# Optimization experiments

Hardware: AMD Instinct MI355X
Metric: run time of the kernel (lower is better)

Reference implementation:

```python
import jax, jax.numpy as jnp
import numpy as np

N, E, IN, H, C, OUT = 50000, 800000, 128, 4, 32, 40
HID = H * C  # 128


def _layernorm(x, g, b, eps=1e-5):
    mu = x.mean(-1, keepdims=True)
    var = ((x - mu) ** 2).mean(-1, keepdims=True)
    return (x - mu) * jax.lax.rsqrt(var + eps) * g + b


def _gatv2(x, src, dst, Wl, bl, Wr, br, att, bias, heads, ch, concat):
    n = x.shape[0]
    xl = (x @ Wl + bl).reshape(n, heads, ch)  # source-side transform
    xr = (x @ Wr + br).reshape(n, heads, ch)  # target-side transform
    e = jax.nn.leaky_relu(xl[src] + xr[dst], 0.2)          # [E,H,C]
    alpha = jnp.einsum('ehc,hc->eh', e, att)                # [E,H]
    m = jax.ops.segment_max(alpha, dst, num_segments=n)
    m = jnp.where(jnp.isfinite(m), m, 0.0)
    a = jnp.exp(alpha - m[dst])
    denom = jax.ops.segment_sum(a, dst, num_segments=n)
    a = a / (denom[dst] + 1e-16)
    out = jax.ops.segment_sum(xl[src] * a[:, :, None], dst, num_segments=n)  # [N,H,C]
    out = out.reshape(n, heads * ch) if concat else out.mean(1)
    return out + bias


def setup_inputs():
    key = jax.random.key(0)
    ks = jax.random.split(key, 26)
    s = 0.05
    rn = lambda k, sh: jax.random.normal(k, sh, jnp.float32) * s
    inp = {
        'x': jax.random.normal(ks[0], (N, IN), jnp.float32),
        'edge_index': jax.random.randint(ks[1], (2, E), 0, N, jnp.int64),
        'W0': rn(ks[2], (IN, HID)), 'b0': jnp.zeros((HID,), jnp.float32),
        'W1l': rn(ks[3], (IN, HID)), 'b1l': jnp.zeros((HID,), jnp.float32),
        'W1r': rn(ks[4], (IN, HID)), 'b1r': jnp.zeros((HID,), jnp.float32),
        'att1': rn(ks[5], (H, C)), 'bias1': jnp.zeros((HID,), jnp.float32),
        'g1': jnp.ones((HID,), jnp.float32), 'be1': jnp.zeros((HID,), jnp.float32),
        'W2l': rn(ks[6], (HID, HID)), 'b2l': jnp.zeros((HID,), jnp.float32),
        'W2r': rn(ks[7], (HID, HID)), 'b2r': jnp.zeros((HID,), jnp.float32),
        'att2': rn(ks[8], (H, C)), 'bias2': jnp.zeros((HID,), jnp.float32),
        'g2': jnp.ones((HID,), jnp.float32), 'be2': jnp.zeros((HID,), jnp.float32),
        'W3l': rn(ks[9], (HID, OUT)), 'b3l': jnp.zeros((OUT,), jnp.float32),
        'W3r': rn(ks[10], (HID, OUT)), 'b3r': jnp.zeros((OUT,), jnp.float32),
        'att3': rn(ks[11], (1, OUT)), 'bias3': jnp.zeros((OUT,), jnp.float32),
    }
    return inp


def reference(x, edge_index, W0, b0, W1l, b1l, W1r, b1r, att1, bias1, g1, be1,
              W2l, b2l, W2r, b2r, att2, bias2, g2, be2,
              W3l, b3l, W3r, b3r, att3, bias3):
    src, dst = edge_index[0], edge_index[1]
    identity = x @ W0 + b0
    out = _gatv2(x, src, dst, W1l, b1l, W1r, b1r, att1, bias1, H, C, True)
    out = jax.nn.gelu(_layernorm(out, g1, be1), approximate=False)
    x1 = out + identity  # dropout is identity in eval mode
    out = _gatv2(x1, src, dst, W2l, b2l, W2r, b2r, att2, bias2, H, C, True)
    out = jax.nn.gelu(_layernorm(out, g2, be2), approximate=False)
    x2 = out + x1
    return _gatv2(x2, src, dst, W3l, b3l, W3r, b3r, att3, bias3, 1, OUT, False)
```

## Files before the change

### kernel.cpp

```cpp
#include <hip/hip_runtime.h>
#include <hip/hip_bf16.h>

#define NN 50000
#define EE 800000
#define OUTD 40
#define NBUCK 196
#define BCAP 8192
#define ABLKS 400
#define EPB 2000

typedef __attribute__((ext_vector_type(8))) short short8;
typedef __attribute__((ext_vector_type(4))) float floatx4;

__device__ __forceinline__ float bf2f(unsigned short u) {
  union { unsigned int i; float f; } v; v.i = ((unsigned int)u) << 16; return v.f;
}
__device__ __forceinline__ unsigned short f2bf(float f) {
  union { float f; unsigned int i; } v; v.f = f;
  unsigned int x = v.i;
  return (unsigned short)((x + 0x7fffu + ((x >> 16) & 1u)) >> 16);
}
__device__ __forceinline__ float blo(unsigned int u) {
  union { unsigned int i; float f; } v; v.i = u << 16; return v.f;
}
__device__ __forceinline__ float bhi(unsigned int u) {
  union { unsigned int i; float f; } v; v.i = u & 0xffff0000u; return v.f;
}

template <int CTRL>
__device__ __forceinline__ float dpp_add(float x) {
  int y = __builtin_amdgcn_update_dpp(0, __float_as_int(x), CTRL, 0xF, 0xF, true);
  return x + __int_as_float(y);
}

__device__ __forceinline__ float gelu1(float y) {
  float y2 = y * y;
  float z = y * fmaf(0.0356774081f, y2, 0.7978845608f);
  float e = __expf(-2.f * z);
  float r = __builtin_amdgcn_rcpf(1.f + e);
  float th = fmaf(2.f, r, -1.f);
  return y * fmaf(0.5f, th, 0.5f);
}

__device__ __forceinline__ int clampe(int i, int last) {
  int r = i <= last ? i : last;
  return r < 0 ? 0 : r;
}

__device__ __forceinline__ int probe_f32(const void* x) {
  int lane = threadIdx.x & 63;
  unsigned short u = ((const unsigned short*)x)[2 * lane];
  int exf = (u >> 7) & 0xFF;
  unsigned long long b = __ballot((exf >= 100 && exf <= 142) ? 1 : 0);
  return (__popcll(b) >= 48) ? 0 : 1;
}
__device__ __forceinline__ int probe_i64(const void* ei) {
  int lane = threadIdx.x & 63;
  long long v = ((const long long*)ei)[lane];
  unsigned long long b = __ballot((v >= 0 && v < NN) ? 1 : 0);
  return (__popcll(b) >= 48) ? 1 : 0;
}

struct WDesc { const void* W; unsigned short* F; int T; int ncols; };
struct WDescs { WDesc d[7]; int cum[8]; };
struct PCv { const void* s; unsigned short* d; int n; int cap; };
struct PCvs { PCv a[17]; };

struct GSet { const unsigned short* F; const unsigned short* bias; unsigned short* Out; };
struct GArgs { GSet s[3]; };

__device__ __forceinline__ short8 pack_f4(float4 u0, float4 u1) {
  short8 r;
  r[0] = (short)f2bf(u0.x); r[1] = (short)f2bf(u0.y);
  r[2] = (short)f2bf(u0.z); r[3] = (short)f2bf(u0.w);
  r[4] = (short)f2bf(u1.x); r[5] = (short)f2bf(u1.y);
  r[6] = (short)f2bf(u1.z); r[7] = (short)f2bf(u1.w);
  return r;
}

__device__ __forceinline__ void gemm_body(int wave, int lane, const void* __restrict__ A,
                                          int f32, const GArgs& g, int nset, int M,
                                          int T, int ncols) {
  int r0 = wave * 16;
  if (r0 >= M) return;
  int m = lane & 15, quad = lane >> 4;
  short8 a0, a1, a2, a3;
  if (!f32) {
    const unsigned short* ar = (const unsigned short*)A + (size_t)(r0 + m) * 128 + quad * 8;
    a0 = *(const short8*)(ar);
    a1 = *(const short8*)(ar + 32);
    a2 = *(const short8*)(ar + 64);
    a3 = *(const short8*)(ar + 96);
  } else {
    const float* ar = (const float*)A + (size_t)(r0 + m) * 128 + quad * 8;
    a0 = pack_f4(*(const float4*)(ar), *(const float4*)(ar + 4));
    a1 = pack_f4(*(const float4*)(ar + 32), *(const float4*)(ar + 36));
    a2 = pack_f4(*(const float4*)(ar + 64), *(const float4*)(ar + 68));
    a3 = pack_f4(*(const float4*)(ar + 96), *(const float4*)(ar + 100));
  }
  size_t kstride = (size_t)T * 64 * 8;
  for (int si = 0; si < nset; ++si) {
    const unsigned short* F = g.s[si].F;
    const unsigned short* bias = g.s[si].bias;
    unsigned short* Out = g.s[si].Out;
    for (int t = 0; t < T; ++t) {
      floatx4 acc = {0.f, 0.f, 0.f, 0.f};
      const unsigned short* wp = F + ((size_t)t * 64 + lane) * 8;
      acc = __builtin_amdgcn_mfma_f32_16x16x32_bf16(a0, *(const short8*)(wp), acc, 0, 0, 0);
      acc = __builtin_amdgcn_mfma_f32_16x16x32_bf16(a1, *(const short8*)(wp + kstride), acc, 0, 0, 0);
      acc = __builtin_amdgcn_mfma_f32_16x16x32_bf16(a2, *(const short8*)(wp + 2 * kstride), acc, 0, 0, 0);
      acc = __builtin_amdgcn_mfma_f32_16x16x32_bf16(a3, *(const short8*)(wp + 3 * kstride), acc, 0, 0, 0);
      int col = t * 16 + m;
      if (col < ncols) {
        float bb = bf2f(bias[col]);
        for (int r = 0; r < 4; ++r) {
          int row = r0 + quad * 4 + r;
          Out[(size_t)row * ncols + col] = f2bf(acc[r] + bb);
        }
      }
    }
  }
}

__global__ __launch_bounds__(512) void fused_scatter_init(
    const void* __restrict__ ei, const void* __restrict__ x,
    unsigned int* __restrict__ bedges, int* __restrict__ bcur,
    int* __restrict__ flags, WDescs ds, PCvs P) {
  __shared__ int lhist[NBUCK];
  __shared__ int lbase[NBUCK];
  if (blockIdx.x >= ABLKS) {
    int b = blockIdx.x - ABLKS;
    int tid = threadIdx.x;
    int f32 = probe_f32(x);
    if (b < 24) {
      int idx = b * 512 + tid;
      if (idx >= 12288) return;
      int mi = 0;
      while (idx >= ds.cum[mi + 1]) mi++;
      int local = idx - ds.cum[mi];
      WDesc d = ds.d[mi];
      int lane = local & 63;
      int rest = local >> 6;
      int t = rest % d.T;
      int kb = rest / d.T;
      int m = lane & 15, quad = lane >> 4;
      int col = t * 16 + m;
      short8 v;
      for (int j = 0; j < 8; ++j) {
        int k = kb * 32 + quad * 8 + j;
        if (col < d.ncols) {
          int off = k * d.ncols + col;
          v[j] = f32 ? (short)f2bf(((const float*)d.W)[off])
                     : (short)((const unsigned short*)d.W)[off];
        } else {
          v[j] = 0;
        }
      }
      *(short8*)(d.F + (size_t)local * 8) = v;
    } else if (b < 41) {
      PCv p = P.a[b - 24];
      for (int i = tid; i < p.cap; i += 512) {
        unsigned short o = 0;
        if (i < p.n)
          o = f32 ? f2bf(((const float*)p.s)[i]) : ((const unsigned short*)p.s)[i];
        p.d[i] = o;
      }
    } else {
      if (tid < 64) {
        int i64 = probe_i64(ei);
        if (tid == 0) {
          flags[0] = i64;
          flags[1] = f32;
          flags[2] = 0;
        }
      }
    }
    return;
  }
  int tid = threadIdx.x;
  if (tid < NBUCK) lhist[tid] = 0;
  int i64 = probe_i64(ei);
  __syncthreads();
  int e0 = blockIdx.x * EPB;
  int e1 = e0 + EPB; if (e1 > EE) e1 = EE;
  for (int e = e0 + tid; e < e1; e += 512) {
    int d = i64 ? (int)((const long long*)ei)[EE + e] : ((const int*)ei)[EE + e];
    d = d < 0 ? 0 : (d >= NN ? NN - 1 : d);
    atomicAdd(&lhist[d >> 8], 1);
  }
  __syncthreads();
  if (tid < NBUCK) {
    int c = lhist[tid];
    lbase[tid] = c ? atomicAdd(&bcur[tid * 16], c) : 0;
    lhist[tid] = 0;
  }
  __syncthreads();
  for (int e = e0 + tid; e < e1; e += 512) {
    int s, d;
    if (i64) {
      s = (int)((const long long*)ei)[e];
      d = (int)((const long long*)ei)[EE + e];
    } else {
      s = ((const int*)ei)[e];
      d = ((const int*)ei)[EE + e];
    }
    s = s < 0 ? 0 : (s >= NN ? NN - 1 : s);
    d = d < 0 ? 0 : (d >= NN ? NN - 1 : d);
    int bin = d >> 8;
    int r = atomicAdd(&lhist[bin], 1);
    int pos = lbase[bin] + r;
    if (pos < BCAP)
      bedges[(size_t)bin * BCAP + pos] =
          ((unsigned int)(d & 0xFF) << 24) | ((unsigned int)s << 8);
  }
}

__global__ __launch_bounds__(512) void fused_sort_gemm(
    const unsigned int* __restrict__ bedges, const int* __restrict__ bcur,
    int* __restrict__ offs, int* __restrict__ src_sorted,
    const void* __restrict__ A, const int* __restrict__ flagp, GArgs g,
    int nset, int M, int T, int ncols) {
  __shared__ int lhist[256];
  __shared__ int lscan[256];
  __shared__ int lbin[256];
  __shared__ int sbase, scount, stotal;
  __shared__ unsigned int le[BCAP];
  __shared__ unsigned short lrank[BCAP];
  if (blockIdx.x >= NBUCK) {
    int wave = (blockIdx.x - NBUCK) * 8 + (threadIdx.x >> 6);
    gemm_body(wave, threadIdx.x & 63, A, *flagp, g, nset, M, T, ncols);
    return;
  }
  int k = blockIdx.x;
  int tid = threadIdx.x;
  if (tid < 256) {
    int c = 0;
    if (tid < NBUCK) {
      int v = bcur[tid * 16];
      c = v < BCAP ? v : BCAP;
    }
    lscan[tid] = c;
  }
  __syncthreads();
  for (int off = 1; off < 256; off <<= 1) {
    int u = 0;
    if (tid < 256 && tid >= off) u = lscan[tid - off];
    __syncthreads();
    if (tid < 256) lscan[tid] += u;
    __syncthreads();
  }
  if (tid == 0) {
    int pb = (k == 0) ? 0 : lscan[k - 1];
    sbase = pb;
    scount = lscan[k] - pb;
    stotal = lscan[NBUCK - 1];
  }
  if (tid < 256) lhist[tid] = 0;
  __syncthreads();
  int base = sbase, count = scount;
  const unsigned int* myb = bedges + (size_t)k * BCAP;
  for (int i = tid; i < count; i += 512) {
    unsigned int pk = myb[i];
    int bin = pk >> 24;
    int r = atomicAdd(&lhist[bin], 1);
    le[i] = pk;
    lrank[i] = (unsigned short)r;
  }
  __syncthreads();
  int hc = 0;
  if (tid < 256) {
    hc = lhist[tid];
    lscan[tid] = hc;
  }
  __syncthreads();
  for (int off = 1; off < 256; off <<= 1) {
    int u = 0;
    if (tid < 256 && tid >= off) u = lscan[tid - off];
    __syncthreads();
    if (tid < 256) lscan[tid] += u;
    __syncthreads();
  }
  if (tid < 256) {
    int binoff = lscan[tid] - hc;
    lbin[tid] = binoff;
    int node = k * 256 + tid;
    if (node < NN) offs[node] = base + binoff;
    if (k == 0 && tid == 0) offs[NN] = stotal;
  }
  __syncthreads();
  for (int i = tid; i < count; i += 512) {
    unsigned int pk = le[i];
    int bin = pk >> 24;
    int pos = base + lbin[bin] + (int)lrank[i];
    src_sorted[pos] = (int)(pk & 0x00FFFF00u);
  }
}

template <int TT, int NCOLS, int WRITEX>
__global__ __launch_bounds__(512) void edge_hid_kernel(
    const unsigned short* __restrict__ xl, const unsigned short* __restrict__ xr,
    const unsigned short* __restrict__ att, const unsigned short* __restrict__ bias,
    const unsigned short* __restrict__ gamma, const unsigned short* __restrict__ beta,
    const unsigned short* __restrict__ resid, unsigned short* __restrict__ xout,
    const int* __restrict__ offs, const int* __restrict__ srcs,
    const unsigned short* __restrict__ Fl, const unsigned short* __restrict__ Fr,
    const unsigned short* __restrict__ bl, const unsigned short* __restrict__ br,
    unsigned short* __restrict__ outl, unsigned short* __restrict__ outr) {
  __shared__ unsigned short sA[16 * 136];
  const int wid = threadIdx.x >> 6;
  int wpair = blockIdx.x * 8 + wid;
  int lane = threadIdx.x & 63;
  int half = lane >> 5;
  int wv = wpair * 2 + half;
  int hl = lane & 31;
  int sub = hl >> 4;
  int cb = (hl & 15) * 16;
  int beg = offs[wv], end = offs[wv + 1], last = end - 1;
  int iters = (end - beg + 1) >> 1;
  int oi = __shfl_xor(iters, 32);
  int maxit = __builtin_amdgcn_readfirstlane(iters > oi ? iters : oi);
  const char* xlb = (const char*)xl;
  int c0 = hl * 4;
  uint2 rr = *(const uint2*)(resid + (size_t)wv * 128 + c0);
  uint4 xr8 = *(const uint4*)((const char*)xr + (size_t)wv * 256 + cb);
  float rx0 = blo(xr8.x), rx1 = bhi(xr8.x), rx2 = blo(xr8.y), rx3 = bhi(xr8.y);
  float rx4 = blo(xr8.z), rx5 = bhi(xr8.z), rx6 = blo(xr8.w), rx7 = bhi(xr8.w);
  uint4 at8 = *(const uint4*)((const char*)att + cb);
  float a0 = blo(at8.x), a1 = bhi(at8.x), a2 = blo(at8.y), a3 = bhi(at8.y);
  float a4 = blo(at8.z), a5 = bhi(at8.z), a6 = blo(at8.w), a7 = bhi(at8.w);
  float acc0 = 0.f, acc1 = 0.f, acc2 = 0.f, acc3 = 0.f;
  float acc4 = 0.f, acc5 = 0.f, acc6 = 0.f, acc7 = 0.f, den = 0.f;
  int ir = beg + sub;
  int o_cur = srcs[clampe(ir, last)];
  int o_nxt = srcs[clampe(ir + 2, last)];
  uint4 u = *(const uint4*)(xlb + (o_cur + cb));
  for (int it = 0; it < maxit; ++it) {
    int o_p = srcs[clampe(ir + 4, last)];
    uint4 un = *(const uint4*)(xlb + (o_nxt + cb));
    float mk = (ir <= last) ? 1.f : 0.f;
    ir += 2;
    float x0 = blo(u.x), x1 = bhi(u.x), x2 = blo(u.y), x3 = bhi(u.y);
    float x4 = blo(u.z), x5 = bhi(u.z), x6 = blo(u.w), x7 = bhi(u.w);
    float t0 = x0 + rx0, t1 = x1 + rx1, t2 = x2 + rx2, t3 = x3 + rx3;
    float t4 = x4 + rx4, t5 = x5 + rx5, t6 = x6 + rx6, t7 = x7 + rx7;
    float pa = a0 * t0;
    pa = fmaf(a1, t1, pa); pa = fmaf(a2, t2, pa); pa = fmaf(a3, t3, pa);
    pa = fmaf(a4, t4, pa); pa = fmaf(a5, t5, pa); pa = fmaf(a6, t6, pa); pa = fmaf(a7, t7, pa);
    float pb = a0 * fabsf(t0);
    pb = fmaf(a1, fabsf(t1), pb); pb = fmaf(a2, fabsf(t2), pb); pb = fmaf(a3, fabsf(t3), pb);
    pb = fmaf(a4, fabsf(t4), pb); pb = fmaf(a5, fabsf(t5), pb);
    pb = fmaf(a6, fabsf(t6), pb); pb = fmaf(a7, fabsf(t7), pb);
    float p = fmaf(0.4f, pb, 0.6f * pa);
    p = dpp_add<0xB1>(p);
    p = dpp_add<0x4E>(p);
    float w = __expf(fminf(p, 60.f)) * mk;
    den += w;
    acc0 = fmaf(w, x0, acc0); acc1 = fmaf(w, x1, acc1);
    acc2 = fmaf(w, x2, acc2); acc3 = fmaf(w, x3, acc3);
    acc4 = fmaf(w, x4, acc4); acc5 = fmaf(w, x5, acc5);
    acc6 = fmaf(w, x6, acc6); acc7 = fmaf(w, x7, acc7);
    u = un;
    o_nxt = o_p;
  }
  den += __shfl_xor(den, 16);
  acc0 += __shfl_xor(acc0, 16); acc1 += __shfl_xor(acc1, 16);
  acc2 += __shfl_xor(acc2, 16); acc3 += __shfl_xor(acc3, 16);
  acc4 += __shfl_xor(acc4, 16); acc5 += __shfl_xor(acc5, 16);
  acc6 += __shfl_xor(acc6, 16); acc7 += __shfl_xor(acc7, 16);
  int srcLane = (half << 5) + (hl >> 1);
  float b0 = __shfl(acc0, srcLane), b1 = __shfl(acc1, srcLane);
  float b2 = __shfl(acc2, srcLane), b3 = __shfl(acc3, srcLane);
  float h4 = __shfl(acc4, srcLane), h5 = __shfl(acc5, srcLane);
  float h6 = __shfl(acc6, srcLane), h7 = __shfl(acc7, srcLane);
  float dn = __shfl(den, srcLane);
  bool hi = (hl & 1) != 0;
  float v0 = hi ? h4 : b0, v1 = hi ? h5 : b1, v2 = hi ? h6 : b2, v3 = hi ? h7 : b3;
  float inv = __builtin_amdgcn_rcpf(dn + 1e-16f);
  uint2 bb = *(const uint2*)(bias + c0);
  float o0 = v0 * inv + blo(bb.x), o1 = v1 * inv + bhi(bb.x);
  float o2 = v2 * inv + blo(bb.y), o3 = v3 * inv + bhi(bb.y);
  float s = (o0 + o1) + (o2 + o3);
  for (int k = 1; k < 32; k <<= 1) s += __shfl_xor(s, k);
  float mu = s * (1.f / 128.f);
  float d0 = o0 - mu, d1 = o1 - mu, d2 = o2 - mu, d3 = o3 - mu;
  float q = (d0 * d0 + d1 * d1) + (d2 * d2 + d3 * d3);
  for (int k = 1; k < 32; k <<= 1) q += __shfl_xor(q, k);
  float rstd = rsqrtf(q * (1.f / 128.f) + 1e-5f);
  uint2 gg = *(const uint2*)(gamma + c0);
  uint2 be = *(const uint2*)(beta + c0);
  float y0 = d0 * rstd * blo(gg.x) + blo(be.x);
  float y1 = d1 * rstd * bhi(gg.x) + bhi(be.x);
  float y2 = d2 * rstd * blo(gg.y) + blo(be.y);
  float y3 = d3 * rstd * bhi(gg.y) + bhi(be.y);
  y0 = gelu1(y0); y1 = gelu1(y1); y2 = gelu1(y2); y3 = gelu1(y3);
  y0 += blo(rr.x); y1 += bhi(rr.x); y2 += blo(rr.y); y3 += bhi(rr.y);
  uint2 pk;
  pk.x = (unsigned int)f2bf(y0) | ((unsigned int)f2bf(y1) << 16);
  pk.y = (unsigned int)f2bf(y2) | ((unsigned int)f2bf(y3) << 16);
  if (WRITEX) *(uint2*)(xout + (size_t)wv * 128 + c0) = pk;

  int lrow = wid * 2 + half;
  *(uint2*)(&sA[lrow * 136 + c0]) = pk;
  __syncthreads();
  int m = lane & 15, quad = lane >> 4;
  const unsigned short* arow = sA + m * 136 + quad * 8;
  short8 A0 = *(const short8*)(arow);
  short8 A1 = *(const short8*)(arow + 32);
  short8 A2 = *(const short8*)(arow + 64);
  short8 A3 = *(const short8*)(arow + 96);
  const size_t kst = (size_t)TT * 64 * 8;
  const int rowbase = blockIdx.x * 16;
  constexpr int PER = (2 * TT) / 8;
#pragma unroll
  for (int jj = 0; jj < PER; ++jj) {
    int j = wid * PER + jj;
    bool isr = j >= TT;
    const unsigned short* F = isr ? Fr : Fl;
    const unsigned short* bs = isr ? br : bl;
    unsigned short* Out = isr ? outr : outl;
    int t = isr ? j - TT : j;
    floatx4 acc = {0.f, 0.f, 0.f, 0.f};
    const unsigned short* wp = F + ((size_t)t * 64 + lane) * 8;
    acc = __builtin_amdgcn_mfma_f32_16x16x32_bf16(A0, *(const short8*)(wp), acc, 0, 0, 0);
    acc = __builtin_amdgcn_mfma_f32_16x16x32_bf16(A1, *(const short8*)(wp + kst), acc, 0, 0, 0);
    acc = __builtin_amdgcn_mfma_f32_16x16x32_bf16(A2, *(const short8*)(wp + 2 * kst), acc, 0, 0, 0);
    acc = __builtin_amdgcn_mfma_f32_16x16x32_bf16(A3, *(const short8*)(wp + 3 * kst), acc, 0, 0, 0);
    int col = t * 16 + m;
    float bbv = bf2f(bs[col]);
#pragma unroll
    for (int r = 0; r < 4; ++r)
      Out[(size_t)(rowbase + quad * 4 + r) * NCOLS + col] = f2bf(acc[r] + bbv);
  }
}

__global__ __launch_bounds__(256) void edge_out_kernel(
    const unsigned short* __restrict__ xl, const unsigned short* __restrict__ xr,
    const unsigned short* __restrict__ att, const unsigned short* __restrict__ bias,
    void* __restrict__ out, const int* __restrict__ flagp,
    const int* __restrict__ offs, const int* __restrict__ srcs) {
  int wv = blockIdx.x * 4 + (threadIdx.x >> 6);
  if (wv >= NN) return;
  int lane = threadIdx.x & 63;
  int oct = lane >> 3;
  int cb = (lane & 7) * 16;
  int beg = __builtin_amdgcn_readfirstlane(offs[wv]);
  int last = __builtin_amdgcn_readfirstlane(offs[wv + 1]) - 1;
  const char* xlb = (const char*)xl;
  uint4 xr8 = *(const uint4*)((const char*)xr + (size_t)wv * 128 + cb);
  float rx0 = blo(xr8.x), rx1 = bhi(xr8.x), rx2 = blo(xr8.y), rx3 = bhi(xr8.y);
  float rx4 = blo(xr8.z), rx5 = bhi(xr8.z), rx6 = blo(xr8.w), rx7 = bhi(xr8.w);
  uint4 at8 = *(const uint4*)((const char*)att + cb);
  float a0 = blo(at8.x), a1 = bhi(at8.x), a2 = blo(at8.y), a3 = bhi(at8.y);
  float a4 = blo(at8.z), a5 = bhi(at8.z), a6 = blo(at8.w), a7 = bhi(at8.w);
  float acc0 = 0.f, acc1 = 0.f, acc2 = 0.f, acc3 = 0.f;
  float acc4 = 0.f, acc5 = 0.f, acc6 = 0.f, acc7 = 0.f, den = 0.f;
  int ir = beg + oct;
  int o_cur = srcs[clampe(ir, last)];
  int o_nxt = srcs[clampe(ir + 8, last)];
  uint4 u = *(const uint4*)(xlb + ((o_cur >> 1) + cb));
  for (int e = beg; e <= last; e += 8) {
    int o_p = srcs[clampe(ir + 16, last)];
    uint4 un = *(const uint4*)(xlb + ((o_nxt >> 1) + cb));
    float mk = (ir <= last) ? 1.f : 0.f;
    ir += 8;
    float x0 = blo(u.x), x1 = bhi(u.x), x2 = blo(u.y), x3 = bhi(u.y);
    float x4 = blo(u.z), x5 = bhi(u.z), x6 = blo(u.w), x7 = bhi(u.w);
    float t0 = x0 + rx0, t1 = x1 + rx1, t2 = x2 + rx2, t3 = x3 + rx3;
    float t4 = x4 + rx4, t5 = x5 + rx5, t6 = x6 + rx6, t7 = x7 + rx7;
    float pa = a0 * t0;
    pa = fmaf(a1, t1, pa); pa = fmaf(a2, t2, pa); pa = fmaf(a3, t3, pa);
    pa = fmaf(a4, t4, pa); pa = fmaf(a5, t5, pa); pa = fmaf(a6, t6, pa); pa = fmaf(a7, t7, pa);
    float pb = a0 * fabsf(t0);
    pb = fmaf(a1, fabsf(t1), pb); pb = fmaf(a2, fabsf(t2), pb); pb = fmaf(a3, fabsf(t3), pb);
    pb = fmaf(a4, fabsf(t4), pb); pb = fmaf(a5, fabsf(t5), pb);
    pb = fmaf(a6, fabsf(t6), pb); pb = fmaf(a7, fabsf(t7), pb);
    float p = fmaf(0.4f, pb, 0.6f * pa);
    p = dpp_add<0xB1>(p);
    p = dpp_add<0x4E>(p);
    p = dpp_add<0x141>(p);
    float w = __expf(fminf(p, 60.f)) * mk;
    den += w;
    acc0 = fmaf(w, x0, acc0); acc1 = fmaf(w, x1, acc1);
    acc2 = fmaf(w, x2, acc2); acc3 = fmaf(w, x3, acc3);
    acc4 = fmaf(w, x4, acc4); acc5 = fmaf(w, x5, acc5);
    acc6 = fmaf(w, x6, acc6); acc7 = fmaf(w, x7, acc7);
    u = un;
    o_nxt = o_p;
  }
  den += __shfl_xor(den, 8);  den += __shfl_xor(den, 16);  den += __shfl_xor(den, 32);
  acc0 += __shfl_xor(acc0, 8); acc0 += __shfl_xor(acc0, 16); acc0 += __shfl_xor(acc0, 32);
  acc1 += __shfl_xor(acc1, 8); acc1 += __shfl_xor(acc1, 16); acc1 += __shfl_xor(acc1, 32);
  acc2 += __shfl_xor(acc2, 8); acc2 += __shfl_xor(acc2, 16); acc2 += __shfl_xor(acc2, 32);
  acc3 += __shfl_xor(acc3, 8); acc3 += __shfl_xor(acc3, 16); acc3 += __shfl_xor(acc3, 32);
  acc4 += __shfl_xor(acc4, 8); acc4 += __shfl_xor(acc4, 16); acc4 += __shfl_xor(acc4, 32);
  acc5 += __shfl_xor(acc5, 8); acc5 += __shfl_xor(acc5, 16); acc5 += __shfl_xor(acc5, 32);
  acc6 += __shfl_xor(acc6, 8); acc6 += __shfl_xor(acc6, 16); acc6 += __shfl_xor(acc6, 32);
  acc7 += __shfl_xor(acc7, 8); acc7 += __shfl_xor(acc7, 16); acc7 += __shfl_xor(acc7, 32);
  float inv = __builtin_amdgcn_rcpf(den + 1e-16f);
  if (lane < 5) {
    uint4 bb = *(const uint4*)((const char*)bias + cb);
    float v0 = acc0 * inv + blo(bb.x), v1 = acc1 * inv + bhi(bb.x);
    float v2 = acc2 * inv + blo(bb.y), v3 = acc3 * inv + bhi(bb.y);
    float v4 = acc4 * inv + blo(bb.z), v5 = acc5 * inv + bhi(bb.z);
    float v6 = acc6 * inv + blo(bb.w), v7 = acc7 * inv + bhi(bb.w);
    int c0 = lane * 8;
    if (*flagp) {
      float* op = (float*)out + (size_t)wv * OUTD + c0;
      float4 f0 = {v0, v1, v2, v3};
      float4 f1 = {v4, v5, v6, v7};
      *(float4*)(op) = f0;
      *(float4*)(op + 4) = f1;
    } else {
      uint4 pk;
      pk.x = (unsigned int)f2bf(v0) | ((unsigned int)f2bf(v1) << 16);
      pk.y = (unsigned int)f2bf(v2) | ((unsigned int)f2bf(v3) << 16);
      pk.z = (unsigned int)f2bf(v4) | ((unsigned int)f2bf(v5) << 16);
      pk.w = (unsigned int)f2bf(v6) | ((unsigned int)f2bf(v7) << 16);
      *(uint4*)((unsigned short*)out + (size_t)wv * OUTD + c0) = pk;
    }
  }
}

extern "C" void kernel_launch(void* const* d_in, const int* in_sizes, int n_in,
                              void* d_out, int out_size, void* d_ws, size_t ws_size,
                              hipStream_t stream) {
  const void* x = d_in[0];
  const void* ei = d_in[1];

  char* ws = (char*)d_ws;
  size_t o = 0;
  auto alloc = [&](size_t bytes) {
    void* p = ws + o;
    o = (o + bytes + 255) & ~(size_t)255;
    return p;
  };
  int* flags = (int*)alloc(256);
  int* src_sorted = (int*)alloc((size_t)EE * 4);
  int* offs = (int*)alloc((size_t)(NN + 1) * 4);
  int* bcur = (int*)alloc((size_t)NBUCK * 16 * 4);
  unsigned int* bedges = (unsigned int*)alloc((size_t)NBUCK * BCAP * 4);
  unsigned short* F_W0 = (unsigned short*)alloc(2048 * 16);
  unsigned short* F_W1l = (unsigned short*)alloc(2048 * 16);
  unsigned short* F_W1r = (unsigned short*)alloc(2048 * 16);
  unsigned short* F_W2l = (unsigned short*)alloc(2048 * 16);
  unsigned short* F_W2r = (unsigned short*)alloc(2048 * 16);
  unsigned short* F_W3l = (unsigned short*)alloc(1024 * 16);
  unsigned short* F_W3r = (unsigned short*)alloc(1024 * 16);
  unsigned short* pblk = (unsigned short*)alloc(4096);
  unsigned short* ident = (unsigned short*)alloc((size_t)NN * 128 * 2);
  unsigned short* bxlA = (unsigned short*)alloc((size_t)NN * 128 * 2);
  unsigned short* bxrA = (unsigned short*)alloc((size_t)NN * 128 * 2);
  unsigned short* bxlB = (unsigned short*)alloc((size_t)NN * 128 * 2);
  unsigned short* bxrB = (unsigned short*)alloc((size_t)NN * 128 * 2);
  (void)ws_size;

  unsigned short* pb0 = pblk;
  unsigned short* pb1l = pblk + 128;
  unsigned short* pb1r = pblk + 256;
  unsigned short* patt1 = pblk + 384;
  unsigned short* pbias1 = pblk + 512;
  unsigned short* pg1 = pblk + 640;
  unsigned short* pbe1 = pblk + 768;
  unsigned short* pb2l = pblk + 896;
  unsigned short* pb2r = pblk + 1024;
  unsigned short* patt2 = pblk + 1152;
  unsigned short* pbias2 = pblk + 1280;
  unsigned short* pg2 = pblk + 1408;
  unsigned short* pbe2 = pblk + 1536;
  unsigned short* pb3l = pblk + 1664;
  unsigned short* pb3r = pblk + 1728;
  unsigned short* patt3 = pblk + 1792;
  unsigned short* pbias3 = pblk + 1856;

  WDescs wd;
  wd.d[0] = {d_in[2], F_W0, 8, 128};
  wd.d[1] = {d_in[4], F_W1l, 8, 128};
  wd.d[2] = {d_in[6], F_W1r, 8, 128};
  wd.d[3] = {d_in[12], F_W2l, 8, 128};
  wd.d[4] = {d_in[14], F_W2r, 8, 128};
  wd.d[5] = {d_in[20], F_W3l, 4, 40};
  wd.d[6] = {d_in[22], F_W3r, 4, 40};
  int cum[8] = {0, 2048, 4096, 6144, 8192, 10240, 11264, 12288};
  for (int i = 0; i < 8; ++i) wd.cum[i] = cum[i];
  PCvs P;
  P.a[0] = {d_in[3], pb0, 128, 128};
  P.a[1] = {d_in[5], pb1l, 128, 128};
  P.a[2] = {d_in[7], pb1r, 128, 128};
  P.a[3] = {d_in[8], patt1, 128, 128};
  P.a[4] = {d_in[9], pbias1, 128, 128};
  P.a[5] = {d_in[10], pg1, 128, 128};
  P.a[6] = {d_in[11], pbe1, 128, 128};
  P.a[7] = {d_in[13], pb2l, 128, 128};
  P.a[8] = {d_in[15], pb2r, 128, 128};
  P.a[9] = {d_in[16], patt2, 128, 128};
  P.a[10] = {d_in[17], pbias2, 128, 128};
  P.a[11] = {d_in[18], pg2, 128, 128};
  P.a[12] = {d_in[19], pbe2, 128, 128};
  P.a[13] = {d_in[21], pb3l, 40, 64};
  P.a[14] = {d_in[23], pb3r, 40, 64};
  P.a[15] = {d_in[24], patt3, 40, 64};
  P.a[16] = {d_in[25], pbias3, 40, 64};

  const int* fx = flags + 1;
  const int gb8 = (NN + 127) / 128;
  const int eb = (NN + 3) / 4;
  const int eb16 = NN / 16;

  hipMemsetAsync(bcur, 0, (size_t)NBUCK * 16 * 4, stream);

  fused_scatter_init<<<ABLKS + 42, 512, 0, stream>>>(ei, x, bedges, bcur, flags, wd, P);

  GArgs g1a;
  g1a.s[0] = {F_W0, pb0, ident};
  g1a.s[1] = {F_W1l, pb1l, bxlA};
  g1a.s[2] = {F_W1r, pb1r, bxrA};
  fused_sort_gemm<<<NBUCK + gb8, 512, 0, stream>>>(bedges, bcur, offs, src_sorted, x,
                                                   fx, g1a, 3, NN, 8, 128);

  edge_hid_kernel<8, 128, 1><<<eb16, 512, 0, stream>>>(
      bxlA, bxrA, patt1, pbias1, pg1, pbe1, ident, ident, offs, src_sorted,
      F_W2l, F_W2r, pb2l, pb2r, bxlB, bxrB);

  edge_hid_kernel<4, 64, 0><<<eb16, 512, 0, stream>>>(
      bxlB, bxrB, patt2, pbias2, pg2, pbe2, ident, ident, offs, src_sorted,
      F_W3l, F_W3r, pb3l, pb3r, bxlA, bxrA);

  edge_out_kernel<<<eb, 256, 0, stream>>>(bxlA, bxrA, patt3, pbias3, d_out, fx, offs,
                                          src_sorted);
}
```

Before: 288.1 us.

## Merge all stages into one cooperative persistent kernel with grid syncs

Replaces five separate kernel launches with a single cooperative mega-kernel that loops over virtual blocks for each phase and separates the phases with grid-wide syncs. Shared memory becomes a union across phases, and the per-bucket capacity is lowered so the larger union fits and more blocks can be resident. The goal is to remove launch gaps and tail effects between stages. In exchange it adds grid-sync cost, puts one shared-memory footprint on every phase, and the smaller bucket capacity could overflow if destination degrees are skewed. The edge-output phase now maps 8 waves per virtual block instead of 4.

```diff
diff --git a/kernel.cpp b/kernel.cpp
--- a/kernel.cpp
+++ b/kernel.cpp
@@ -1,13 +1,21 @@
 #include <hip/hip_runtime.h>
 #include <hip/hip_bf16.h>
+#include <hip/hip_cooperative_groups.h>
+
+namespace cg = cooperative_groups;
 
 #define NN 50000
 #define EE 800000
 #define OUTD 40
 #define NBUCK 196
-#define BCAP 8192
+#define BCAP 4608
 #define ABLKS 400
 #define EPB 2000
+#define GB8 391
+#define NV1 (ABLKS + 42)
+#define NV2 (NBUCK + GB8)
+#define NV3 (NN / 16)
+#define NV5 (NN / 8)
 
 typedef __attribute__((ext_vector_type(8))) short short8;
 typedef __attribute__((ext_vector_type(4))) float floatx4;
@@ -65,9 +73,34 @@
 struct WDescs { WDesc d[7]; int cum[8]; };
 struct PCv { const void* s; unsigned short* d; int n; int cap; };
 struct PCvs { PCv a[17]; };
-
 struct GSet { const unsigned short* F; const unsigned short* bias; unsigned short* Out; };
 struct GArgs { GSet s[3]; };
+
+union SharedU {
+  struct { int lhist[NBUCK]; int lbase[NBUCK]; } s1;
+  struct {
+    int lhist[256]; int lscan[256]; int lbin[256];
+    int sbase, scount, stotal;
+    unsigned int le[BCAP];
+    unsigned short lrank[BCAP];
+  } s2;
+  unsigned short sA[16 * 136];
+};
+
+struct MegaArgs {
+  const void* x; const void* ei;
+  unsigned int* bedges; int* bcur; int* flags;
+  int* offs; int* srcs;
+  WDescs wd; PCvs P;
+  GArgs g1;
+  const unsigned short *patt1, *pbias1, *pg1, *pbe1;
+  const unsigned short *patt2, *pbias2, *pg2, *pbe2;
+  const unsigned short *patt3, *pbias3;
+  const unsigned short *F2l, *F2r, *b2l, *b2r;
+  const unsigned short *F3l, *F3r, *b3l, *b3r;
+  unsigned short *ident, *bxlA, *bxrA, *bxlB, *bxrB;
+  void* out;
+};
 
 __device__ __forceinline__ short8 pack_f4(float4 u0, float4 u1) {
   short8 r;
@@ -78,9 +111,8 @@
   return r;
 }
 
-__device__ __forceinline__ void gemm_body(int wave, int lane, const void* __restrict__ A,
-                                          int f32, const GArgs& g, int nset, int M,
-                                          int T, int ncols) {
+__device__ void gemm_body(int wave, int lane, const void* __restrict__ A,
+                          int f32, const GArgs& g, int nset, int M, int T, int ncols) {
   int r0 = wave * 16;
   if (r0 >= M) return;
   int m = lane & 15, quad = lane >> 4;
@@ -122,23 +154,18 @@
   }
 }
 
-__global__ __launch_bounds__(512) void fused_scatter_init(
-    const void* __restrict__ ei, const void* __restrict__ x,
-    unsigned int* __restrict__ bedges, int* __restrict__ bcur,
-    int* __restrict__ flags, WDescs ds, PCvs P) {
-  __shared__ int lhist[NBUCK];
-  __shared__ int lbase[NBUCK];
-  if (blockIdx.x >= ABLKS) {
-    int b = blockIdx.x - ABLKS;
+__device__ void phase_scatter_init(int vb, SharedU& su, const MegaArgs& a) {
+  if (vb >= ABLKS) {
+    int b = vb - ABLKS;
     int tid = threadIdx.x;
-    int f32 = probe_f32(x);
+    int f32 = probe_f32(a.x);
     if (b < 24) {
       int idx = b * 512 + tid;
       if (idx >= 12288) return;
       int mi = 0;
-      while (idx >= ds.cum[mi + 1]) mi++;
-      int local = idx - ds.cum[mi];
-      WDesc d = ds.d[mi];
+      while (idx >= a.wd.cum[mi + 1]) mi++;
+      int local = idx - a.wd.cum[mi];
+      WDesc d = a.wd.d[mi];
       int lane = local & 63;
       int rest = local >> 6;
       int t = rest % d.T;
@@ -158,7 +185,7 @@
       }
       *(short8*)(d.F + (size_t)local * 8) = v;
     } else if (b < 41) {
-      PCv p = P.a[b - 24];
+      PCv p = a.P.a[b - 24];
       for (int i = tid; i < p.cap; i += 512) {
         unsigned short o = 0;
         if (i < p.n)
@@ -167,32 +194,33 @@
       }
     } else {
       if (tid < 64) {
-        int i64 = probe_i64(ei);
+        int i64 = probe_i64(a.ei);
         if (tid == 0) {
-          flags[0] = i64;
-          flags[1] = f32;
-          flags[2] = 0;
+          a.flags[0] = i64;
+          a.flags[1] = f32;
+          a.flags[2] = 0;
         }
       }
     }
     return;
   }
   int tid = threadIdx.x;
-  if (tid < NBUCK) lhist[tid] = 0;
-  int i64 = probe_i64(ei);
-  __syncthreads();
-  int e0 = blockIdx.x * EPB;
+  if (tid < NBUCK) su.s1.lhist[tid] = 0;
+  int i64 = probe_i64(a.ei);
+  __syncthreads();
+  int e0 = vb * EPB;
   int e1 = e0 + EPB; if (e1 > EE) e1 = EE;
+  const void* ei = a.ei;
   for (int e = e0 + tid; e < e1; e += 512) {
     int d = i64 ? (int)((const long long*)ei)[EE + e] : ((const int*)ei)[EE + e];
     d = d < 0 ? 0 : (d >= NN ? NN - 1 : d);
-    atomicAdd(&lhist[d >> 8], 1);
+    atomicAdd(&su.s1.lhist[d >> 8], 1);
   }
   __syncthreads();
   if (tid < NBUCK) {
-    int c = lhist[tid];
-    lbase[tid] = c ? atomicAdd(&bcur[tid * 16], c) : 0;
-    lhist[tid] = 0;
+    int c = su.s1.lhist[tid];
+    su.s1.lbase[tid] = c ? atomicAdd(&a.bcur[tid * 16], c) : 0;
+    su.s1.lhist[tid] = 0;
   }
   __syncthreads();
   for (int e = e0 + tid; e < e1; e += 512) {
@@ -207,108 +235,107 @@
     s = s < 0 ? 0 : (s >= NN ? NN - 1 : s);
     d = d < 0 ? 0 : (d >= NN ? NN - 1 : d);
     int bin = d >> 8;
-    int r = atomicAdd(&lhist[bin], 1);
-    int pos = lbase[bin] + r;
+    int r = atomicAdd(&su.s1.lhist[bin], 1);
+    int pos = su.s1.lbase[bin] + r;
     if (pos < BCAP)
-      bedges[(size_t)bin * BCAP + pos] =
+      a.bedges[(size_t)bin * BCAP + pos] =
           ((unsigned int)(d & 0xFF) << 24) | ((unsigned int)s << 8);
   }
-}
-
-__global__ __launch_bounds__(512) void fused_sort_gemm(
-    const unsigned int* __restrict__ bedges, const int* __restrict__ bcur,
-    int* __restrict__ offs, int* __restrict__ src_sorted,
-    const void* __restrict__ A, const int* __restrict__ flagp, GArgs g,
-    int nset, int M, int T, int ncols) {
-  __shared__ int lhist[256];
-  __shared__ int lscan[256];
-  __shared__ int lbin[256];
-  __shared__ int sbase, scount, stotal;
-  __shared__ unsigned int le[BCAP];
-  __shared__ unsigned short lrank[BCAP];
-  if (blockIdx.x >= NBUCK) {
-    int wave = (blockIdx.x - NBUCK) * 8 + (threadIdx.x >> 6);
-    gemm_body(wave, threadIdx.x & 63, A, *flagp, g, nset, M, T, ncols);
+  __syncthreads();
+}
+
+__device__ void phase_sort_gemm(int vb, SharedU& su, const MegaArgs& a) {
+  if (vb >= NBUCK) {
+    int wave = (vb - NBUCK) * 8 + (threadIdx.x >> 6);
+    gemm_body(wave, threadIdx.x & 63, a.x, a.flags[1], a.g1, 3, NN, 8, 128);
     return;
   }
-  int k = blockIdx.x;
+  auto& s = su.s2;
+  int k = vb;
   int tid = threadIdx.x;
   if (tid < 256) {
     int c = 0;
     if (tid < NBUCK) {
-      int v = bcur[tid * 16];
+      int v = a.bcur[tid * 16];
       c = v < BCAP ? v : BCAP;
     }
-    lscan[tid] = c;
+    s.lscan[tid] = c;
   }
   __syncthreads();
   for (int off = 1; off < 256; off <<= 1) {
     int u = 0;
-    if (tid < 256 && tid >= off) u = lscan[tid - off];
+    if (tid < 256 && tid >= off) u = s.lscan[tid - off];
     __syncthreads();
-    if (tid < 256) lscan[tid] += u;
+    if (tid < 256) s.lscan[tid] += u;
     __syncthreads();
   }
   if (tid == 0) {
-    int pb = (k == 0) ? 0 : lscan[k - 1];
-    sbase = pb;
-    scount = lscan[k] - pb;
-    stotal = lscan[NBUCK - 1];
-  }
-  if (tid < 256) lhist[tid] = 0;
-  __syncthreads();
-  int base = sbase, count = scount;
-  const unsigned int* myb = bedges + (size_t)k * BCAP;
+    int pb = (k == 0) ? 0 : s.lscan[k - 1];
+    s.sbase = pb;
+    s.scount = s.lscan[k] - pb;
+    s.stotal = s.lscan[NBUCK - 1];
+  }
+  if (tid < 256) s.lhist[tid] = 0;
+  __syncthreads();
+  int base = s.sbase, count = s.scount;
+  const unsigned int* myb = a.bedges + (size_t)k * BCAP;
   for (int i = tid; i < count; i += 512) {
     unsigned int pk = myb[i];
     int bin = pk >> 24;
-    int r = atomicAdd(&lhist[bin], 1);
-    le[i] = pk;
-    lrank[i] = (unsigned short)r;
+    int r = atomicAdd(&s.lhist[bin], 1);
+    s.le[i] = pk;
+    s.lrank[i] = (unsigned short)r;
   }
   __syncthreads();
   int hc = 0;
   if (tid < 256) {
-    hc = lhist[tid];
-    lscan[tid] = hc;
+    hc = s.lhist[tid];
+    s.lscan[tid] = hc;
   }
   __syncthreads();
   for (int off = 1; off < 256; off <<= 1) {
     int u = 0;
-    if (tid < 256 && tid >= off) u = lscan[tid - off];
+    if (tid < 256 && tid >= off) u = s.lscan[tid - off];
     __syncthreads();
-    if (tid < 256) lscan[tid] += u;
+    if (tid < 256) s.lscan[tid] += u;
     __syncthreads();
   }
   if (tid < 256) {
-    int binoff = lscan[tid] - hc;
-    lbin[tid] = binoff;
+    int binoff = s.lscan[tid] - hc;
+    s.lbin[tid] = binoff;
     int node = k * 256 + tid;
-    if (node < NN) offs[node] = base + binoff;
-    if (k == 0 && tid == 0) offs[NN] = stotal;
+    if (node < NN) a.offs[node] = base + binoff;
+    if (k == 0 && tid == 0) a.offs[NN] = s.stotal;
   }
   __syncthreads();
   for (int i = tid; i < count; i += 512) {
-    unsigned int pk = le[i];
+    unsigned int pk = s.le[i];
     int bin = pk >> 24;
-    int pos = base + lbin[bin] + (int)lrank[i];
-    src_sorted[pos] = (int)(pk & 0x00FFFF00u);
+    int pos = base + s.lbin[bin] + (int)s.lrank[i];
+    a.srcs[pos] = (int)(pk & 0x00FFFF00u);
   }
 }
 
 template <int TT, int NCOLS, int WRITEX>
-__global__ __launch_bounds__(512) void edge_hid_kernel(
-    const unsigned short* __restrict__ xl, const unsigned short* __restrict__ xr,
-    const unsigned short* __restrict__ att, const unsigned short* __restrict__ bias,
-    const unsigned short* __restrict__ gamma, const unsigned short* __restrict__ beta,
-    const unsigned short* __restrict__ resid, unsigned short* __restrict__ xout,
-    const int* __restrict__ offs, const int* __restrict__ srcs,
-    const unsigned short* __restrict__ Fl, const unsigned short* __restrict__ Fr,
-    const unsigned short* __restrict__ bl, const unsigned short* __restrict__ br,
-    unsigned short* __restrict__ outl, unsigned short* __restrict__ outr) {
-  __shared__ unsigned short sA[16 * 136];
+__device__ void eh_body(int vb, SharedU& su,
+                        const unsigned short* __restrict__ xl,
+                        const unsigned short* __restrict__ xr,
+                        const unsigned short* __restrict__ att,
+                        const unsigned short* __restrict__ bias,
+                        const unsigned short* __restrict__ gamma,
+                        const unsigned short* __restrict__ beta,
+                        const unsigned short* __restrict__ resid,
+                        unsigned short* __restrict__ xout,
+                        const int* __restrict__ offs, const int* __restrict__ srcs,
+                        const unsigned short* __restrict__ Fl,
+                        const unsigned short* __restrict__ Fr,
+                        const unsigned short* __restrict__ bl,
+                        const unsigned short* __restrict__ br,
+                        unsigned short* __restrict__ outl,
+                        unsigned short* __restrict__ outr) {
+  unsigned short* sA = su.sA;
   const int wid = threadIdx.x >> 6;
-  int wpair = blockIdx.x * 8 + wid;
+  int wpair = vb * 8 + wid;
   int lane = threadIdx.x & 63;
   int half = lane >> 5;
   int wv = wpair * 2 + half;
@@ -408,8 +435,9 @@
   short8 A1 = *(const short8*)(arow + 32);
   short8 A2 = *(const short8*)(arow + 64);
   short8 A3 = *(const short8*)(arow + 96);
+  __syncthreads();
   const size_t kst = (size_t)TT * 64 * 8;
-  const int rowbase = blockIdx.x * 16;
+  const int rowbase = vb * 16;
   constexpr int PER = (2 * TT) / 8;
 #pragma unroll
   for (int jj = 0; jj < PER; ++jj) {
@@ -433,12 +461,14 @@
   }
 }
 
-__global__ __launch_bounds__(256) void edge_out_kernel(
-    const unsigned short* __restrict__ xl, const unsigned short* __restrict__ xr,
-    const unsigned short* __restrict__ att, const unsigned short* __restrict__ bias,
-    void* __restrict__ out, const int* __restrict__ flagp,
-    const int* __restrict__ offs, const int* __restrict__ srcs) {
-  int wv = blockIdx.x * 4 + (threadIdx.x >> 6);
+__device__ void eout_body(int vb,
+                          const unsigned short* __restrict__ xl,
+                          const unsigned short* __restrict__ xr,
+                          const unsigned short* __restrict__ att,
+                          const unsigned short* __restrict__ bias,
+                          void* __restrict__ out, const int* __restrict__ flagp,
+                          const int* __restrict__ offs, const int* __restrict__ srcs) {
+  int wv = vb * 8 + (threadIdx.x >> 6);
   if (wv >= NN) return;
   int lane = threadIdx.x & 63;
   int oct = lane >> 3;
@@ -521,6 +551,29 @@
   }
 }
 
+__global__ __launch_bounds__(512) void mega_kernel(MegaArgs a) {
+  __shared__ SharedU su;
+  cg::grid_group grid = cg::this_grid();
+  const int nb = gridDim.x;
+  for (int vb = blockIdx.x; vb < NV1; vb += nb) phase_scatter_init(vb, su, a);
+  grid.sync();
+  for (int vb = blockIdx.x; vb < NV2; vb += nb) phase_sort_gemm(vb, su, a);
+  grid.sync();
+  for (int vb = blockIdx.x; vb < NV3; vb += nb)
+    eh_body<8, 128, 1>(vb, su, a.bxlA, a.bxrA, a.patt1, a.pbias1, a.pg1, a.pbe1,
+                       a.ident, a.ident, a.offs, a.srcs,
+                       a.F2l, a.F2r, a.b2l, a.b2r, a.bxlB, a.bxrB);
+  grid.sync();
+  for (int vb = blockIdx.x; vb < NV3; vb += nb)
+    eh_body<4, 64, 0>(vb, su, a.bxlB, a.bxrB, a.patt2, a.pbias2, a.pg2, a.pbe2,
+                      a.ident, a.ident, a.offs, a.srcs,
+                      a.F3l, a.F3r, a.b3l, a.b3r, a.bxlA, a.bxrA);
+  grid.sync();
+  for (int vb = blockIdx.x; vb < NV5; vb += nb)
+    eout_body(vb, a.bxlA, a.bxrA, a.patt3, a.pbias3, a.out, a.flags + 1,
+              a.offs, a.srcs);
+}
+
 extern "C" void kernel_launch(void* const* d_in, const int* in_sizes, int n_in,
                               void* d_out, int out_size, void* d_ws, size_t ws_size,
                               hipStream_t stream) {
@@ -572,59 +625,54 @@
   unsigned short* patt3 = pblk + 1792;
   unsigned short* pbias3 = pblk + 1856;
 
-  WDescs wd;
-  wd.d[0] = {d_in[2], F_W0, 8, 128};
-  wd.d[1] = {d_in[4], F_W1l, 8, 128};
-  wd.d[2] = {d_in[6], F_W1r, 8, 128};
-  wd.d[3] = {d_in[12], F_W2l, 8, 128};
-  wd.d[4] = {d_in[14], F_W2r, 8, 128};
-  wd.d[5] = {d_in[20], F_W3l, 4, 40};
-  wd.d[6] = {d_in[22], F_W3r, 4, 40};
+  MegaArgs ma;
+  ma.x = x; ma.ei = ei;
+  ma.bedges = bedges; ma.bcur = bcur; ma.flags = flags;
+  ma.offs = offs; ma.srcs = src_sorted;
+  ma.wd.d[0] = {d_in[2], F_W0, 8, 128};
+  ma.wd.d[1] = {d_in[4], F_W1l, 8, 128};
+  ma.wd.d[2] = {d_in[6], F_W1r, 8, 128};
+  ma.wd.d[3] = {d_in[12], F_W2l, 8, 128};
+  ma.wd.d[4] = {d_in[14], F_W2r, 8, 128};
+  ma.wd.d[5] = {d_in[20], F_W3l, 4, 40};
+  ma.wd.d[6] = {d_in[22], F_W3r, 4, 40};
   int cum[8] = {0, 2048, 4096, 6144, 8192, 10240, 11264, 12288};
-  for (int i = 0; i < 8; ++i) wd.cum[i] = cum[i];
-  PCvs P;
-  P.a[0] = {d_in[3], pb0, 128, 128};
-  P.a[1] = {d_in[5], pb1l, 128, 128};
-  P.a[2] = {d_in[7], pb1r, 128, 128};
-  P.a[3] = {d_in[8], patt1, 128, 128};
-  P.a[4] = {d_in[9], pbias1, 128, 128};
-  P.a[5] = {d_in[10], pg1, 128, 128};
-  P.a[6] = {d_in[11], pbe1, 128, 128};
-  P.a[7] = {d_in[13], pb2l, 128, 128};
-  P.a[8] = {d_in[15], pb2r, 128, 128};
-  P.a[9] = {d_in[16], patt2, 128, 128};
-  P.a[10] = {d_in[17], pbias2, 128, 128};
-  P.a[11] = {d_in[18], pg2, 128, 128};
-  P.a[12] = {d_in[19], pbe2, 128, 128};
-  P.a[13] = {d_in[21], pb3l, 40, 64};
-  P.a[14] = {d_in[23], pb3r, 40, 64};
-  P.a[15] = {d_in[24], patt3, 40, 64};
-  P.a[16] = {d_in[25], pbias3, 40, 64};
-
-  const int* fx = flags + 1;
-  const int gb8 = (NN + 127) / 128;
-  const int eb = (NN + 3) / 4;
-  const int eb16 = NN / 16;
+  for (int i = 0; i < 8; ++i) ma.wd.cum[i] = cum[i];
+  ma.P.a[0] = {d_in[3], pb0, 128, 128};
+  ma.P.a[1] = {d_in[5], pb1l, 128, 128};
+  ma.P.a[2] = {d_in[7], pb1r, 128, 128};
+  ma.P.a[3] = {d_in[8], patt1, 128, 128};
+  ma.P.a[4] = {d_in[9], pbias1, 128, 128};
+  ma.P.a[5] = {d_in[10], pg1, 128, 128};
+  ma.P.a[6] = {d_in[11], pbe1, 128, 128};
+  ma.P.a[7] = {d_in[13], pb2l, 128, 128};
+  ma.P.a[8] = {d_in[15], pb2r, 128, 128};
+  ma.P.a[9] = {d_in[16], patt2, 128, 128};
+  ma.P.a[10] = {d_in[17], pbias2, 128, 128};
+  ma.P.a[11] = {d_in[18], pg2, 128, 128};
+  ma.P.a[12] = {d_in[19], pbe2, 128, 128};
+  ma.P.a[13] = {d_in[21], pb3l, 40, 64};
+  ma.P.a[14] = {d_in[23], pb3r, 40, 64};
+  ma.P.a[15] = {d_in[24], patt3, 40, 64};
+  ma.P.a[16] = {d_in[25], pbias3, 40, 64};
+  ma.g1.s[0] = {F_W0, pb0, ident};
+  ma.g1.s[1] = {F_W1l, pb1l, bxlA};
+  ma.g1.s[2] = {F_W1r, pb1r, bxrA};
+  ma.patt1 = patt1; ma.pbias1 = pbias1; ma.pg1 = pg1; ma.pbe1 = pbe1;
+  ma.patt2 = patt2; ma.pbias2 = pbias2; ma.pg2 = pg2; ma.pbe2 = pbe2;
+  ma.patt3 = patt3; ma.pbias3 = pbias3;
+  ma.F2l = F_W2l; ma.F2r = F_W2r; ma.b2l = pb2l; ma.b2r = pb2r;
+  ma.F3l = F_W3l; ma.F3r = F_W3r; ma.b3l = pb3l; ma.b3r = pb3r;
+  ma.ident = ident; ma.bxlA = bxlA; ma.bxrA = bxrA; ma.bxlB = bxlB; ma.bxrB = bxrB;
+  ma.out = d_out;
 
   hipMemsetAsync(bcur, 0, (size_t)NBUCK * 16 * 4, stream);
 
-  fused_scatter_init<<<ABLKS + 42, 512, 0, stream>>>(ei, x, bedges, bcur, flags, wd, P);
-
-  GArgs g1a;
-  g1a.s[0] = {F_W0, pb0, ident};
-  g1a.s[1] = {F_W1l, pb1l, bxlA};
-  g1a.s[2] = {F_W1r, pb1r, bxrA};
-  fused_sort_gemm<<<NBUCK + gb8, 512, 0, stream>>>(bedges, bcur, offs, src_sorted, x,
-                                                   fx, g1a, 3, NN, 8, 128);
-
-  edge_hid_kernel<8, 128, 1><<<eb16, 512, 0, stream>>>(
-      bxlA, bxrA, patt1, pbias1, pg1, pbe1, ident, ident, offs, src_sorted,
-      F_W2l, F_W2r, pb2l, pb2r, bxlB, bxrB);
-
-  edge_hid_kernel<4, 64, 0><<<eb16, 512, 0, stream>>>(
-      bxlB, bxrB, patt2, pbias2, pg2, pbe2, ident, ident, offs, src_sorted,
-      F_W3l, F_W3r, pb3l, pb3r, bxlA, bxrA);
-
-  edge_out_kernel<<<eb, 256, 0, stream>>>(bxlA, bxrA, patt3, pbias3, d_out, fx, offs,
-                                          src_sorted);
-}
+  int maxb = 0;
+  hipOccupancyMaxActiveBlocksPerMultiprocessor(&maxb, (const void*)mega_kernel, 512, 0);
+  if (maxb < 1) maxb = 1;
+  if (maxb > 4) maxb = 4;
+  void* kp[] = {&ma};
+  hipLaunchCooperativeKernel((const void*)mega_kernel, dim3(maxb * 256), dim3(512),
+                             kp, 0, stream);
+}
```

After: 645.4 us. 124% more time.
